# Performance work log

Hardware: AMD Instinct MI355X
Metric: run time of the kernel (lower is better)

## Reference

```python
import jax, jax.numpy as jnp
import numpy as np

N = 25000
E = 400000
HIDDEN = 512
NH = 8
DH = HIDDEN // NH


def setup_inputs() -> dict:
    key = jax.random.key(0)
    ks = jax.random.split(key, 10)
    s = 1.0 / np.sqrt(HIDDEN)
    return {
        "h": jax.random.normal(ks[0], (N, HIDDEN), dtype=jnp.float32),
        "Wq": jax.random.normal(ks[1], (HIDDEN, HIDDEN), dtype=jnp.float32) * s,
        "bq": jnp.zeros((HIDDEN,), dtype=jnp.float32),
        "Wk": jax.random.normal(ks[2], (HIDDEN, HIDDEN), dtype=jnp.float32) * s,
        "bk": jnp.zeros((HIDDEN,), dtype=jnp.float32),
        "Wo": jax.random.normal(ks[3], (HIDDEN, HIDDEN), dtype=jnp.float32) * s,
        "bo": jnp.zeros((HIDDEN,), dtype=jnp.float32),
        "rows": jax.random.randint(ks[4], (E,), 0, N, dtype=jnp.int32),
        "cols": jax.random.randint(ks[5], (E,), 0, N, dtype=jnp.int32),
    }


def reference(h, Wq, bq, Wk, bk, Wo, bo, rows, cols):
    # Projections; reshape (N, dh, nh) exactly as the source does.
    q = (h @ Wq + bq).reshape(N, DH, NH)
    k = (h @ Wk + bk).reshape(N, DH, NH)
    v = k  # source bug kept faithfully: v = linear_k(h)

    # SDDMM: per-edge, per-head dot product (no 1/sqrt(dh) scaling in source).
    scores = jnp.einsum("edh,edh->eh", q[rows], k[cols])  # [E, NH]

    # Row-wise (source-node) segment softmax per head.
    m = jax.ops.segment_max(scores, rows, num_segments=N)       # [N, NH]
    ex = jnp.exp(scores - m[rows])                              # [E, NH]
    denom = jax.ops.segment_sum(ex, rows, num_segments=N)      # [N, NH]
    attn = ex / denom[rows]                                     # [E, NH]

    # SpMM: out[i] = sum_{j in nbr(i)} attn[ij] * v[j]
    msgs = attn[:, None, :] * v[cols]                           # [E, DH, NH]
    out = jax.ops.segment_sum(msgs, rows, num_segments=N)      # [N, DH, NH]

    return out.reshape(N, HIDDEN) @ Wo + bo
```

## Files before the change

kernel.cpp:

```cpp
#include <hip/hip_runtime.h>
#include <math.h>

typedef unsigned short u16;
typedef unsigned int u32;
typedef __attribute__((ext_vector_type(8))) _Float16 half8;
typedef __attribute__((ext_vector_type(2))) _Float16 half2v;
typedef __attribute__((ext_vector_type(8))) u16 ushort8;
typedef __attribute__((ext_vector_type(4))) float f32x4;

__device__ __forceinline__ u16 f2h(float f) {
    union { u16 u; _Float16 h; } c; c.h = (_Float16)f; return c.u;
}

#if __has_builtin(__builtin_amdgcn_fdot2)
#define FDOT2(a, b, c) __builtin_amdgcn_fdot2((a), (b), (c), false)
#else
#define FDOT2(a, b, c) fmaf((float)(a)[0], (float)(b)[0], \
                        fmaf((float)(a)[1], (float)(b)[1], (c)))
#endif

__device__ __forceinline__ void gload16(void* lds, const void* g) {
    __builtin_amdgcn_global_load_lds(
        (const __attribute__((address_space(1))) u32*)g,
        (__attribute__((address_space(3))) u32*)lds,
        16, 0, 0);
}

template <int OUTMODE>
__device__ __forceinline__ void gemm_body(
    const u16* A, const u16* Bp, const float* bias, void* Cout, int Mout,
    int m0, int colBase, u16* As0, u16* As1, u16* Bs0, u16* Bs1)
{
    const int tid  = threadIdx.x;
    const int wave = tid >> 6;
    const int lane = tid & 63;
    const int wr = (wave >> 1) * 64;
    const int wc = (wave & 1) * 128;

    f32x4 acc[4][8];
#pragma unroll
    for (int i = 0; i < 4; ++i)
#pragma unroll
        for (int j = 0; j < 8; ++j) acc[i][j] = (f32x4){0.f, 0.f, 0.f, 0.f};

    const int srow  = lane >> 2;
    const int scolG = ((lane & 3) ^ ((srow >> 1) & 3)) * 8;
    const size_t gOffA = (size_t)(m0 + wave * 32 + srow) * 512 + scolG;
    const size_t gOffB = (size_t)(wave * 64 + srow) * 512 + scolG;
    const int lOffA = wave * 1024 + srow * 32 + (lane & 3) * 8;
    const int lOffB = wave * 2048 + srow * 32 + (lane & 3) * 8;

    const int fR = ((lane & 15) >> 1) & 3;
    const int paOff = (wr + (lane & 15)) * 32 + ((lane >> 4) ^ fR) * 8;
    const int pbOff = (wc + (lane & 15)) * 32 + ((lane >> 4) ^ fR) * 8;

    auto STAGE = [&](u16* sa, u16* sb, int ko) {
        gload16(sa + lOffA,        A  + gOffA + ko);
        gload16(sa + lOffA + 512,  A  + gOffA + ko + 16 * 512);
        gload16(sb + lOffB,        Bp + gOffB + ko);
        gload16(sb + lOffB + 512,  Bp + gOffB + ko + 16 * 512);
        gload16(sb + lOffB + 1024, Bp + gOffB + ko + 32 * 512);
        gload16(sb + lOffB + 1536, Bp + gOffB + ko + 48 * 512);
    };
    auto COMPUTE = [&](const u16* sa, const u16* sb) {
        half8 af[4], bf[8];
#pragma unroll
        for (int i = 0; i < 4; ++i) af[i] = *(const half8*)(sa + paOff + i * 512);
#pragma unroll
        for (int j = 0; j < 8; ++j) bf[j] = *(const half8*)(sb + pbOff + j * 512);
#pragma unroll
        for (int i = 0; i < 4; ++i)
#pragma unroll
            for (int j = 0; j < 8; ++j)
                acc[i][j] = __builtin_amdgcn_mfma_f32_16x16x32_f16(
                    af[i], bf[j], acc[i][j], 0, 0, 0);
    };

    STAGE(As0, Bs0, 0);
    __syncthreads();
#pragma unroll
    for (int kt = 0; kt < 16; kt += 2) {
        STAGE(As1, Bs1, (kt + 1) * 32);
        COMPUTE(As0, Bs0);
        __syncthreads();
        if (kt + 2 < 16) STAGE(As0, Bs0, (kt + 2) * 32);
        COMPUTE(As1, Bs1);
        __syncthreads();
    }

    const int ccolL = wc + (lane & 15);
    const int crow0 = m0 + wr + (lane >> 4) * 4;
#pragma unroll
    for (int j = 0; j < 8; ++j) {
        const float b = bias[ccolL + j * 16];
        const int col = colBase + ccolL + j * 16;
#pragma unroll
        for (int i = 0; i < 4; ++i) {
#pragma unroll
            for (int r = 0; r < 4; ++r) {
                int row = crow0 + i * 16 + r;
                if (row < Mout) {
                    float v = acc[i][j][r] + b;
                    size_t off = (size_t)row * 512 + col;
                    if (OUTMODE == 0) ((float*)Cout)[off] = v;
                    else              ((u16*)Cout)[off] = f2h(v);
                }
            }
        }
    }
}

__global__ __launch_bounds__(256) void gemm_qk(
    const u16* __restrict__ hh, const u16* __restrict__ Wqt,
    const u16* __restrict__ Wkt, const float* __restrict__ bqp,
    const float* __restrict__ bkp, u16* __restrict__ Qh,
    u16* __restrict__ Kb, int nPad)
{
    const int bid = blockIdx.x;
    const int m = (bid >> 5) * 8 + (bid & 7);
    const int s = (bid >> 3) & 3;
    if (m >= nPad / 128) return;
    const int z = s >> 1;
    const int nloc = (s & 1) * 256;

    __shared__ __align__(16) u16 As0[4096], As1[4096], Bs0[8192], Bs1[8192];
    const u16* Bp = (z ? Wkt : Wqt) + (size_t)nloc * 512;
    const float* bp = (z ? bkp : bqp) + nloc;
    u16* out = z ? Kb : Qh;
    gemm_body<1>(hh, Bp, bp, out, nPad, m * 128, nloc, As0, As1, Bs0, Bs1);
}

__global__ __launch_bounds__(256) void gemm_wo(
    const u16* __restrict__ A, const u16* __restrict__ Wot,
    const float* __restrict__ bo, float* __restrict__ C, int Mout, int nPad)
{
    const int bid = blockIdx.x;
    const int m = (bid >> 4) * 8 + (bid & 7);
    const int s = (bid >> 3) & 1;
    if (m >= nPad / 128) return;
    const int nloc = s * 256;

    __shared__ __align__(16) u16 As0[4096], As1[4096], Bs0[8192], Bs1[8192];
    gemm_body<0>(A, Wot + (size_t)nloc * 512, bo + nloc, C, Mout,
                 m * 128, nloc, As0, As1, Bs0, Bs1);
}

__global__ __launch_bounds__(256) void prep(
    const float* __restrict__ h, u16* __restrict__ hh, int nN,
    const int* __restrict__ rows, int* __restrict__ deg, int E,
    const float* __restrict__ Wq, const float* __restrict__ Wk,
    const float* __restrict__ Wo, const float* __restrict__ bq,
    const float* __restrict__ bk,
    u16* __restrict__ Wqt, u16* __restrict__ Wkt, u16* __restrict__ Wot,
    float* __restrict__ bqp, float* __restrict__ bkp,
    int nbH, int nbE)
{
    __shared__ float T[64][65];
    const int tid = threadIdx.x;
    const int b = blockIdx.x;

    if (b < nbH) {
        int t = b * 256 + tid;
        size_t e = (size_t)t * 8;
        int row = (int)(e >> 9);
        ushort8 o;
        if (row < nN) {
            f32x4 a = *(const f32x4*)(h + e);
            f32x4 bb = *(const f32x4*)(h + e + 4);
            float x[8] = {a.x, a.y, a.z, a.w, bb.x, bb.y, bb.z, bb.w};
#pragma unroll
            for (int i = 0; i < 8; ++i) o[i] = f2h(x[i]);
        } else {
            o = (ushort8){0,0,0,0,0,0,0,0};
        }
        *(ushort8*)(hh + e) = o;
        return;
    }
    if (b < nbH + nbE) {
        int i = (b - nbH) * 256 + tid;
        if (i < E) atomicAdd(&deg[rows[i]], 1);
        return;
    }
    int rem = b - nbH - nbE;
    const int z = rem >> 6;
    const int X = (rem & 7) * 64;
    const int Y = ((rem >> 3) & 7) * 64;

    const int r4 = tid >> 4;
    const int c4 = (tid & 15) * 4;
    if (z < 2) {
        const float* W = z ? Wk : Wq;
#pragma unroll
        for (int rr = 0; rr < 64; rr += 16) {
            f32x4 v = *(const f32x4*)(W + (size_t)(X + rr + r4) * 512 + Y + c4);
            T[rr + r4][c4 + 0] = v.x; T[rr + r4][c4 + 1] = v.y;
            T[rr + r4][c4 + 2] = v.z; T[rr + r4][c4 + 3] = v.w;
        }
    } else {
#pragma unroll
        for (int rr = 0; rr < 64; rr += 16) {
            int p2 = (rr + r4) * 8 + (X >> 6);
            f32x4 v = *(const f32x4*)(Wo + (size_t)p2 * 512 + Y + c4);
            T[rr + r4][c4 + 0] = v.x; T[rr + r4][c4 + 1] = v.y;
            T[rr + r4][c4 + 2] = v.z; T[rr + r4][c4 + 3] = v.w;
        }
    }
    __syncthreads();

    const int cc = tid >> 2;
    const int ks = (tid & 3) * 16;
    const int pc = Y + cc;
    const int ro = (z < 2) ? ((pc & 7) * 64 + (pc >> 3)) : pc;
    ushort8 h0, h1;
#pragma unroll
    for (int t = 0; t < 8; ++t) {
        h0[t] = f2h(T[ks + t][cc]);
        h1[t] = f2h(T[ks + 8 + t][cc]);
    }
    size_t o = (size_t)ro * 512 + X + ks;
    if (z == 0) {
        *(ushort8*)(Wqt + o) = h0; *(ushort8*)(Wqt + o + 8) = h1;
    } else if (z == 1) {
        *(ushort8*)(Wkt + o) = h0; *(ushort8*)(Wkt + o + 8) = h1;
    } else {
        *(ushort8*)(Wot + o) = h0; *(ushort8*)(Wot + o + 8) = h1;
        if (rem == 128) {
            for (int bi = tid; bi < 512; bi += 256) {
                int pp = (bi & 63) * 8 + (bi >> 6);
                bqp[bi] = bq[pp];
                bkp[bi] = bk[pp];
            }
        }
    }
}

#define SCAN_CHUNK 2048

__global__ __launch_bounds__(256) void scan_partial(
    const int* __restrict__ deg, int* __restrict__ bsum, int n)
{
    int base = blockIdx.x * SCAN_CHUNK;
    int t = threadIdx.x;
    int s = 0;
    for (int i = t; i < SCAN_CHUNK; i += 256) {
        int g = base + i;
        s += (g < n) ? deg[g] : 0;
    }
#pragma unroll
    for (int off = 1; off < 64; off <<= 1) s += __shfl_xor(s, off, 64);
    __shared__ int ws[4];
    if ((t & 63) == 0) ws[t >> 6] = s;
    __syncthreads();
    if (t == 0) bsum[blockIdx.x] = ws[0] + ws[1] + ws[2] + ws[3];
}

__global__ __launch_bounds__(256) void scan_final(
    const int* __restrict__ deg, const int* __restrict__ bsum,
    int* __restrict__ rowptr, int* __restrict__ cursor, int n, int nb)
{
    int boff = 0, total = 0;
    for (int i = 0; i < nb; ++i) {
        int v = bsum[i];
        if (i < (int)blockIdx.x) boff += v;
        total += v;
    }
    int t = threadIdx.x;
    int base = blockIdx.x * SCAN_CHUNK + t * 8;
    int v[8];
    int s = 0;
#pragma unroll
    for (int i = 0; i < 8; ++i) {
        int g = base + i;
        v[i] = (g < n) ? deg[g] : 0;
        s += v[i];
    }
    int lane = t & 63, w = t >> 6;
    int inc = s;
#pragma unroll
    for (int off = 1; off < 64; off <<= 1) {
        int x = __shfl_up(inc, off, 64);
        if (lane >= off) inc += x;
    }
    __shared__ int wsum[4];
    if (lane == 63) wsum[w] = inc;
    __syncthreads();
    int excl = boff + inc - s;
    for (int i = 0; i < w; ++i) excl += wsum[i];
#pragma unroll
    for (int i = 0; i < 8; ++i) {
        int g = base + i;
        if (g < n) { rowptr[g] = excl; cursor[g] = excl; }
        excl += v[i];
    }
    if (blockIdx.x == 0 && t == 0) rowptr[n] = total;
}

__global__ void scatter_kernel(const int* __restrict__ rows, const int* __restrict__ cols,
                               int* __restrict__ cursor, int* __restrict__ colc, int E)
{
    int i = blockIdx.x * 256 + threadIdx.x;
    if (i < E) {
        int pos = atomicAdd(&cursor[rows[i]], 1);
        colc[pos] = cols[i];
    }
}

__global__ __launch_bounds__(256) void node_agg(
    const u16* __restrict__ Qh, const u16* __restrict__ Kb,
    const int* __restrict__ rowptr, const int* __restrict__ colc,
    u16* __restrict__ aggb, int nN)
{
    int node = blockIdx.x * 4 + (threadIdx.x >> 6);
    int lane = threadIdx.x & 63;
    if (node >= nN) return;
    size_t base = (size_t)node * 512 + lane * 8;

    half8 qv = __builtin_nontemporal_load((const half8*)(Qh + base));
    half2v q2[4];
#pragma unroll
    for (int i = 0; i < 4; ++i) q2[i] = (half2v){qv[2 * i], qv[2 * i + 1]};

    int start = rowptr[node];
    int deg   = rowptr[node + 1] - start;
    const int* cp = colc + start;
    const size_t loff = (size_t)lane * 8;

    float m = -__builtin_inff();
    float den = 0.f;
    half2v acc2[4];
#pragma unroll
    for (int i = 0; i < 4; ++i) acc2[i] = (half2v){(_Float16)0.f, (_Float16)0.f};

    if (deg > 0) {
        const int dl = deg - 1;
        half8 k[8];
#pragma unroll
        for (int t = 0; t < 8; ++t) {
            int it = t < dl ? t : dl;
            k[t] = *(const half8*)(Kb + (size_t)cp[it] * 512 + loff);
        }
        for (int j = 0; j < deg; j += 8) {
            half8 nx[8];
#pragma unroll
            for (int t = 0; t < 8; ++t) {
                int it = j + 8 + t < dl ? j + 8 + t : dl;
                nx[t] = *(const half8*)(Kb + (size_t)cp[it] * 512 + loff);
            }

            float p[8];
#pragma unroll
            for (int t = 0; t < 8; ++t) {
                float s = 0.f;
#pragma unroll
                for (int i = 0; i < 4; ++i) {
                    half2v bb = (half2v){k[t][2 * i], k[t][2 * i + 1]};
                    s = FDOT2(q2[i], bb, s);
                }
                p[t] = s;
            }
#pragma unroll
            for (int off = 1; off < 8; off <<= 1) {
#pragma unroll
                for (int t = 0; t < 8; ++t) p[t] += __shfl_xor(p[t], off, 64);
            }

            float pm = p[0];
#pragma unroll
            for (int t = 1; t < 8; ++t) pm = fmaxf(pm, p[t]);
            if (__any(pm > m + 4.f)) {
                float mn = fmaxf(m, pm);
                float sc = __expf(m - mn);
                den *= sc;
                _Float16 sch = (_Float16)sc;
                half2v sc2 = {sch, sch};
#pragma unroll
                for (int i = 0; i < 4; ++i) acc2[i] *= sc2;
                m = mn;
            }
#pragma unroll
            for (int t = 0; t < 8; ++t) {
                float w = (j + t < deg) ? __expf(p[t] - m) : 0.f;
                den += w;
                _Float16 wh = (_Float16)w;
                half2v w2 = {wh, wh};
#pragma unroll
                for (int i = 0; i < 4; ++i) {
                    half2v bb = (half2v){k[t][2 * i], k[t][2 * i + 1]};
                    acc2[i] += w2 * bb;
                }
            }
#pragma unroll
            for (int t = 0; t < 8; ++t) k[t] = nx[t];
        }
    }

    float inv = (deg > 0) ? 1.f / den : 0.f;
    ushort8 o;
#pragma unroll
    for (int i = 0; i < 4; ++i) {
        o[2 * i]     = f2h((float)acc2[i][0] * inv);
        o[2 * i + 1] = f2h((float)acc2[i][1] * inv);
    }
    __builtin_nontemporal_store(o, (ushort8*)(aggb + base));
}

extern "C" void kernel_launch(void* const* d_in, const int* in_sizes, int n_in,
                              void* d_out, int out_size, void* d_ws, size_t ws_size,
                              hipStream_t stream)
{
    const float* h  = (const float*)d_in[0];
    const float* Wq = (const float*)d_in[1];
    const float* bq = (const float*)d_in[2];
    const float* Wk = (const float*)d_in[3];
    const float* bk = (const float*)d_in[4];
    const float* Wo = (const float*)d_in[5];
    const float* bo = (const float*)d_in[6];
    const int* rows = (const int*)d_in[7];
    const int* cols = (const int*)d_in[8];
    float* out = (float*)d_out;

    const int HID = 512;
    const int nN  = in_sizes[0] / HID;
    const int E   = in_sizes[7];
    const int nPad = (nN + 127) & ~127;
    const int nb = (nN + SCAN_CHUNK - 1) / SCAN_CHUNK;
    const int nbH = nPad * (HID / 8) / 256;
    const int nbE = (E + 255) / 256;
    const int nMt = nPad / 128;
    const int nGrp = (nMt + 7) / 8;

    char* w = (char*)d_ws;
    u16* Kb  = (u16*)w;  w += (size_t)nPad * HID * 2;
    u16* hh  = (u16*)w;  w += (size_t)nPad * HID * 2;
    u16* Qh  = (u16*)w;  w += (size_t)nPad * HID * 2;
    u16* Wqt = (u16*)w;  w += 512 * 512 * 2;
    u16* Wkt = (u16*)w;  w += 512 * 512 * 2;
    u16* Wot = (u16*)w;  w += 512 * 512 * 2;
    float* bqp = (float*)w;  w += 512 * 4;
    float* bkp = (float*)w;  w += 512 * 4;
    int* rowptr = (int*)w;   w += (size_t)(nN + 1) * 4;
    int* cursor = (int*)w;   w += (size_t)nN * 4;
    int* deg    = (int*)w;   w += (size_t)nN * 4;
    int* bsum   = (int*)w;   w += 64 * 4;
    int* colc   = (int*)w;

    (void)hipMemsetAsync(deg, 0, (size_t)nN * sizeof(int), stream);

    prep<<<nbH + nbE + 192, 256, 0, stream>>>(
        h, hh, nN, rows, deg, E, Wq, Wk, Wo, bq, bk,
        Wqt, Wkt, Wot, bqp, bkp, nbH, nbE);

    scan_partial<<<nb, 256, 0, stream>>>(deg, bsum, nN);
    scan_final<<<nb, 256, 0, stream>>>(deg, bsum, rowptr, cursor, nN, nb);
    scatter_kernel<<<(E + 255) / 256, 256, 0, stream>>>(rows, cols, cursor, colc, E);

    gemm_qk<<<nGrp * 32, 256, 0, stream>>>(
        hh, Wqt, Wkt, bqp, bkp, Qh, Kb, nPad);

    node_agg<<<(nN + 3) / 4, 256, 0, stream>>>(Qh, Kb, rowptr, colc, hh, nN);

    gemm_wo<<<nGrp * 16, 256, 0, stream>>>(hh, Wot, bo, out, nN, nPad);
}
```

Baseline: 233.6 us.

## Use 128x128 GEMM tiles with triple-buffered LDS and fuse edge scatter into QK GEMM

The GEMM tile shrinks from 128x256 to 128x128 per block, and the double-buffered K loop becomes a three-stage LDS ring. Each step waits with a partial vmcnt before a single barrier, so fewer synchronisations are needed and more loads stay in flight. The CSR edge-scatter kernel is folded into the QK GEMM launch as extra blocks, which removes one launch and lets the atomic scatter overlap GEMM work. The smaller tiles double the block count and lower register pressure, at the cost of more redundant A-tile loads.

After: 243.5 us. 4.3% more time.

```diff
diff --git a/kernel.cpp b/kernel.cpp
--- a/kernel.cpp
+++ b/kernel.cpp
@@ -28,72 +28,72 @@
 
 template <int OUTMODE>
 __device__ __forceinline__ void gemm_body(
-    const u16* A, const u16* Bp, const float* bias, void* Cout, int Mout,
-    int m0, int colBase, u16* As0, u16* As1, u16* Bs0, u16* Bs1)
+    const u16* A, const u16* Bt, const float* bias, void* Cout, int Mout,
+    int m0, int n0, u16* AsB, u16* BsB)
 {
     const int tid  = threadIdx.x;
     const int wave = tid >> 6;
     const int lane = tid & 63;
     const int wr = (wave >> 1) * 64;
-    const int wc = (wave & 1) * 128;
-
-    f32x4 acc[4][8];
+    const int wc = (wave & 1) * 64;
+
+    f32x4 acc[4][4];
 #pragma unroll
     for (int i = 0; i < 4; ++i)
 #pragma unroll
-        for (int j = 0; j < 8; ++j) acc[i][j] = (f32x4){0.f, 0.f, 0.f, 0.f};
+        for (int j = 0; j < 4; ++j) acc[i][j] = (f32x4){0.f, 0.f, 0.f, 0.f};
 
     const int srow  = lane >> 2;
     const int scolG = ((lane & 3) ^ ((srow >> 1) & 3)) * 8;
     const size_t gOffA = (size_t)(m0 + wave * 32 + srow) * 512 + scolG;
-    const size_t gOffB = (size_t)(wave * 64 + srow) * 512 + scolG;
-    const int lOffA = wave * 1024 + srow * 32 + (lane & 3) * 8;
-    const int lOffB = wave * 2048 + srow * 32 + (lane & 3) * 8;
+    const size_t gOffB = (size_t)(n0 + wave * 32 + srow) * 512 + scolG;
+    const int lOff = wave * 1024 + srow * 32 + (lane & 3) * 8;
 
     const int fR = ((lane & 15) >> 1) & 3;
     const int paOff = (wr + (lane & 15)) * 32 + ((lane >> 4) ^ fR) * 8;
     const int pbOff = (wc + (lane & 15)) * 32 + ((lane >> 4) ^ fR) * 8;
 
-    auto STAGE = [&](u16* sa, u16* sb, int ko) {
-        gload16(sa + lOffA,        A  + gOffA + ko);
-        gload16(sa + lOffA + 512,  A  + gOffA + ko + 16 * 512);
-        gload16(sb + lOffB,        Bp + gOffB + ko);
-        gload16(sb + lOffB + 512,  Bp + gOffB + ko + 16 * 512);
-        gload16(sb + lOffB + 1024, Bp + gOffB + ko + 32 * 512);
-        gload16(sb + lOffB + 1536, Bp + gOffB + ko + 48 * 512);
+    auto STAGE = [&](int buf, int ko) {
+        u16* sa = AsB + buf * 4096;
+        u16* sb = BsB + buf * 4096;
+        gload16(sa + lOff,       A  + gOffA + ko);
+        gload16(sa + lOff + 512, A  + gOffA + ko + 16 * 512);
+        gload16(sb + lOff,       Bt + gOffB + ko);
+        gload16(sb + lOff + 512, Bt + gOffB + ko + 16 * 512);
     };
-    auto COMPUTE = [&](const u16* sa, const u16* sb) {
-        half8 af[4], bf[8];
+    auto COMPUTE = [&](int buf) {
+        const u16* sa = AsB + buf * 4096;
+        const u16* sb = BsB + buf * 4096;
+        half8 af[4], bf[4];
 #pragma unroll
         for (int i = 0; i < 4; ++i) af[i] = *(const half8*)(sa + paOff + i * 512);
 #pragma unroll
-        for (int j = 0; j < 8; ++j) bf[j] = *(const half8*)(sb + pbOff + j * 512);
+        for (int j = 0; j < 4; ++j) bf[j] = *(const half8*)(sb + pbOff + j * 512);
 #pragma unroll
         for (int i = 0; i < 4; ++i)
 #pragma unroll
-            for (int j = 0; j < 8; ++j)
+            for (int j = 0; j < 4; ++j)
                 acc[i][j] = __builtin_amdgcn_mfma_f32_16x16x32_f16(
                     af[i], bf[j], acc[i][j], 0, 0, 0);
     };
 
-    STAGE(As0, Bs0, 0);
-    __syncthreads();
-#pragma unroll
-    for (int kt = 0; kt < 16; kt += 2) {
-        STAGE(As1, Bs1, (kt + 1) * 32);
-        COMPUTE(As0, Bs0);
-        __syncthreads();
-        if (kt + 2 < 16) STAGE(As0, Bs0, (kt + 2) * 32);
-        COMPUTE(As1, Bs1);
-        __syncthreads();
-    }
-
-    const int ccolL = wc + (lane & 15);
+    STAGE(0, 0);
+    STAGE(1, 32);
+#pragma unroll
+    for (int kt = 0; kt < 16; ++kt) {
+        if (kt < 15) asm volatile("s_waitcnt vmcnt(4)" ::: "memory");
+        else         asm volatile("s_waitcnt vmcnt(0)" ::: "memory");
+        __builtin_amdgcn_s_barrier();
+        __builtin_amdgcn_sched_barrier(0);
+        if (kt + 2 < 16) STAGE((kt + 2) % 3, (kt + 2) * 32);
+        COMPUTE(kt % 3);
+    }
+
+    const int ccol  = n0 + wc + (lane & 15);
     const int crow0 = m0 + wr + (lane >> 4) * 4;
 #pragma unroll
-    for (int j = 0; j < 8; ++j) {
-        const float b = bias[ccolL + j * 16];
-        const int col = colBase + ccolL + j * 16;
+    for (int j = 0; j < 4; ++j) {
+        const float b = bias[ccol + j * 16];
 #pragma unroll
         for (int i = 0; i < 4; ++i) {
 #pragma unroll
@@ -101,7 +101,7 @@
                 int row = crow0 + i * 16 + r;
                 if (row < Mout) {
                     float v = acc[i][j][r] + b;
-                    size_t off = (size_t)row * 512 + col;
+                    size_t off = (size_t)row * 512 + ccol + j * 16;
                     if (OUTMODE == 0) ((float*)Cout)[off] = v;
                     else              ((u16*)Cout)[off] = f2h(v);
                 }
@@ -114,35 +114,43 @@
     const u16* __restrict__ hh, const u16* __restrict__ Wqt,
     const u16* __restrict__ Wkt, const float* __restrict__ bqp,
     const float* __restrict__ bkp, u16* __restrict__ Qh,
-    u16* __restrict__ Kb, int nPad)
+    u16* __restrict__ Kb, int nPad,
+    const int* __restrict__ rows, const int* __restrict__ cols,
+    int* __restrict__ cursor, int* __restrict__ colc, int E, int nGemm)
+{
+    __shared__ __align__(16) u16 AsB[3 * 4096], BsB[3 * 4096];
+    const int bid = blockIdx.x;
+    if (bid >= nGemm) {
+        int i = (bid - nGemm) * 256 + threadIdx.x;
+        if (i < E) {
+            int pos = atomicAdd(&cursor[rows[i]], 1);
+            colc[pos] = cols[i];
+        }
+        return;
+    }
+    const int m = (bid >> 6) * 8 + (bid & 7);
+    const int s = (bid >> 3) & 7;
+    if (m >= nPad / 128) return;
+    const int z = s >> 2;
+    const int n = s & 3;
+
+    const u16* Bt = z ? Wkt : Wqt;
+    const float* bias = z ? bkp : bqp;
+    u16* out = z ? Kb : Qh;
+    gemm_body<1>(hh, Bt, bias, out, nPad, m * 128, n * 128, AsB, BsB);
+}
+
+__global__ __launch_bounds__(256) void gemm_wo(
+    const u16* __restrict__ A, const u16* __restrict__ Wot,
+    const float* __restrict__ bo, float* __restrict__ C, int Mout, int nPad)
 {
     const int bid = blockIdx.x;
     const int m = (bid >> 5) * 8 + (bid & 7);
     const int s = (bid >> 3) & 3;
     if (m >= nPad / 128) return;
-    const int z = s >> 1;
-    const int nloc = (s & 1) * 256;
-
-    __shared__ __align__(16) u16 As0[4096], As1[4096], Bs0[8192], Bs1[8192];
-    const u16* Bp = (z ? Wkt : Wqt) + (size_t)nloc * 512;
-    const float* bp = (z ? bkp : bqp) + nloc;
-    u16* out = z ? Kb : Qh;
-    gemm_body<1>(hh, Bp, bp, out, nPad, m * 128, nloc, As0, As1, Bs0, Bs1);
-}
-
-__global__ __launch_bounds__(256) void gemm_wo(
-    const u16* __restrict__ A, const u16* __restrict__ Wot,
-    const float* __restrict__ bo, float* __restrict__ C, int Mout, int nPad)
-{
-    const int bid = blockIdx.x;
-    const int m = (bid >> 4) * 8 + (bid & 7);
-    const int s = (bid >> 3) & 1;
-    if (m >= nPad / 128) return;
-    const int nloc = s * 256;
-
-    __shared__ __align__(16) u16 As0[4096], As1[4096], Bs0[8192], Bs1[8192];
-    gemm_body<0>(A, Wot + (size_t)nloc * 512, bo + nloc, C, Mout,
-                 m * 128, nloc, As0, As1, Bs0, Bs1);
+
+    __shared__ __align__(16) u16 AsB[3 * 4096], BsB[3 * 4096];
+    gemm_body<0>(A, Wot, bo, C, Mout, m * 128, s * 128, AsB, BsB);
 }
 
 __global__ __launch_bounds__(256) void prep(
@@ -295,16 +303,6 @@
     if (blockIdx.x == 0 && t == 0) rowptr[n] = total;
 }
 
-__global__ void scatter_kernel(const int* __restrict__ rows, const int* __restrict__ cols,
-                               int* __restrict__ cursor, int* __restrict__ colc, int E)
-{
-    int i = blockIdx.x * 256 + threadIdx.x;
-    if (i < E) {
-        int pos = atomicAdd(&cursor[rows[i]], 1);
-        colc[pos] = cols[i];
-    }
-}
-
 __global__ __launch_bounds__(256) void node_agg(
     const u16* __restrict__ Qh, const u16* __restrict__ Kb,
     const int* __restrict__ rowptr, const int* __restrict__ colc,
@@ -428,6 +426,7 @@
     const int nbE = (E + 255) / 256;
     const int nMt = nPad / 128;
     const int nGrp = (nMt + 7) / 8;
+    const int nGemmQK = nGrp * 64;
 
     char* w = (char*)d_ws;
     u16* Kb  = (u16*)w;  w += (size_t)nPad * HID * 2;
@@ -452,12 +451,12 @@
 
     scan_partial<<<nb, 256, 0, stream>>>(deg, bsum, nN);
     scan_final<<<nb, 256, 0, stream>>>(deg, bsum, rowptr, cursor, nN, nb);
-    scatter_kernel<<<(E + 255) / 256, 256, 0, stream>>>(rows, cols, cursor, colc, E);
-
-    gemm_qk<<<nGrp * 32, 256, 0, stream>>>(
-        hh, Wqt, Wkt, bqp, bkp, Qh, Kb, nPad);
+
+    gemm_qk<<<nGemmQK + nbE, 256, 0, stream>>>(
+        hh, Wqt, Wkt, bqp, bkp, Qh, Kb, nPad,
+        rows, cols, cursor, colc, E, nGemmQK);
 
     node_agg<<<(nN + 3) / 4, 256, 0, stream>>>(Qh, Kb, rowptr, colc, hh, nN);
 
-    gemm_wo<<<nGrp * 16, 256, 0, stream>>>(hh, Wot, bo, out, nN, nPad);
-}
+    gemm_wo<<<nGrp * 32, 256, 0, stream>>>(hh, Wot, bo, out, nN, nPad);
+}
```
